# Kernel optimization log

Measured on AMD Instinct MI355X. Metric: run time of the kernel, lower is better.

Reference implementation:

```python
import jax, jax.numpy as jnp
import numpy as np

SIZE_DICT = 1024  # K
DIM_DICT = 256    # D


def setup_inputs() -> dict:
    key = jax.random.key(0)
    k1, k2, k3 = jax.random.split(key, 3)
    z = jax.random.normal(k1, (64, 1024, DIM_DICT), dtype=jnp.float32)
    codebook = jax.random.normal(k2, (SIZE_DICT, DIM_DICT), dtype=jnp.float32)
    codebook_weight = jax.random.normal(k3, (SIZE_DICT,), dtype=jnp.float32)
    return {
        "z_from_encoder": z,
        "codebook": codebook,
        "codebook_weight": codebook_weight,
        "flg_train": 0,
    }


def reference(z_from_encoder, codebook, codebook_weight, flg_train):
    z = z_from_encoder
    z_flat = z.reshape(-1, DIM_DICT)  # [N, D]
    # Pairwise squared distances: ||z||^2 + ||c||^2 - 2 z.c  -> [N, K]
    cost = (
        jnp.sum(z_flat ** 2, axis=1, keepdims=True)
        + jnp.sum(codebook ** 2, axis=1)
        - 2.0 * jnp.matmul(z_flat, codebook.T)
    )
    idx = jnp.argmin(cost, axis=1)  # [N]
    # one-hot scatter + matmul with codebook == gather of codebook rows
    z_q = codebook[idx].reshape(z.shape)
    # straight-through estimator
    z_q = z + jax.lax.stop_gradient(z_q - z)
    # loss is 0.0 in eval (flg_train False)
    loss = jnp.float32(0.0)
    # perplexity from mean one-hot encodings
    n = z_flat.shape[0]
    counts = jnp.zeros((SIZE_DICT,), dtype=jnp.float32).at[idx].add(1.0)
    e_mean = counts / n
    perplexity = jnp.exp(-jnp.sum(e_mean * jnp.log(e_mean + 1e-10)))
    return z_q, loss, perplexity
```

## Files before the change

### kernel.cpp

```cpp
#include <hip/hip_runtime.h>
#include <hip/hip_bf16.h>
#include <stdint.h>


typedef float  v4f __attribute__((ext_vector_type(4)));
typedef _Float16 v8h __attribute__((ext_vector_type(8)));
typedef _Float16 v4h __attribute__((ext_vector_type(4)));

#define N_ROWS 65536
#define N_DICT 1024
#define DIMS   256
#define MARGIN 4e-3f

__device__ __forceinline__ void gl_lds16(const void* g, void* l) {
  __builtin_amdgcn_global_load_lds(
      (const __attribute__((address_space(1))) unsigned int*)g,
      (__attribute__((address_space(3))) unsigned int*)l,
      16, 0, 0);
}

__global__ void k_prep(const float* __restrict__ cb, _Float16* __restrict__ swz_h,
                       _Float16* __restrict__ swz_l, float* __restrict__ cnA,
                       double* __restrict__ cnD,
                       unsigned* __restrict__ hist, unsigned* __restrict__ counters) {
  const int b = blockIdx.x, t = threadIdx.x;
  if (b == 0) {
    for (int i = t; i < N_DICT; i += 256) hist[i] = 0u;
    if (t == 0) { counters[0] = 0u; counters[1] = 0u; }
  }
  const int gid = b * 256 + t;
  const int col = gid >> 6;
  const int k0  = (gid & 63) * 4;
  v4f v = ((const v4f*)cb)[gid];
  v4h h, l;
  #pragma unroll
  for (int j = 0; j < 4; ++j) {
    h[j] = (_Float16)v[j];
    float r = v[j] - (float)h[j];
    l[j] = (_Float16)r;
  }
  const int c = col >> 6, t4 = (col >> 4) & 3, l15 = col & 15;
  const int kk = k0 >> 5, q = (k0 >> 3) & 3, j0 = k0 & 7;
  const size_t off = (size_t)(((c * 8 + kk) * 4 + t4) * 512 + (q * 16 + l15) * 8 + j0);
  *(v4h*)(swz_h + off) = h;
  *(v4h*)(swz_l + off) = l;
  const int lane = t & 63, w = t >> 6;
  const int row = b * 4 + w;
  v4f u = ((const v4f*)cb)[row * 64 + lane];
  double s = (double)u[0]*u[0] + (double)u[1]*u[1]
           + (double)u[2]*u[2] + (double)u[3]*u[3];
  #pragma unroll
  for (int d = 1; d < 64; d <<= 1) s += __shfl_xor(s, d);
  if (lane == 0) { cnA[row] = (float)s; cnD[row] = s; }
}

__launch_bounds__(512, 2)
__global__ void k_main(const float* __restrict__ z, const _Float16* __restrict__ swz_h,
                       const _Float16* __restrict__ swz_l, const float* __restrict__ cnA,
                       unsigned* __restrict__ out_idx,
                       unsigned long long* __restrict__ list1,
                       unsigned* __restrict__ list2,
                       unsigned* __restrict__ counters) {
  __shared__ __align__(16) char lds[4][32768];
  const int t = threadIdx.x, lane = t & 63, w = t >> 6;
  const int l15 = lane & 15, q = lane >> 4;
  const int waverow = (blockIdx.x * 8 + w) * 32;

  v8h ah[2][8], al[2][8];
  #pragma unroll
  for (int m = 0; m < 2; ++m) {
    const float* zp = z + (size_t)(waverow + m * 16 + l15) * DIMS + q * 8;
    #pragma unroll
    for (int kk = 0; kk < 8; ++kk) {
      v4f f0 = *(const v4f*)(zp + kk * 32);
      v4f f1 = *(const v4f*)(zp + kk * 32 + 4);
      v8h hh, ll;
      #pragma unroll
      for (int j = 0; j < 4; ++j) {
        hh[j] = (_Float16)f0[j];
        float r = f0[j] - (float)hh[j];
        ll[j] = (_Float16)r;
        hh[4 + j] = (_Float16)f1[j];
        r = f1[j] - (float)hh[4 + j];
        ll[4 + j] = (_Float16)r;
      }
      ah[m][kk] = hh; al[m][kk] = ll;
    }
  }

  const int s0 = w * 4;
  const char* gsrc_base = (const char*)(s0 >= 16 ? swz_l : swz_h);

  float m1[8], m2[8], m3[8]; int c1[8], c2[8];
  #pragma unroll
  for (int s = 0; s < 8; ++s) {
    m1[s] = 1e30f; m2[s] = 1e30f; m3[s] = 1e30f; c1[s] = 0; c2[s] = 0;
  }

  #pragma unroll
  for (int n = 0; n < 2; ++n) {
    const int c = n >> 1, half = n & 1;
    #pragma unroll
    for (int i = 0; i < 4; ++i) {
      const int s = s0 + i, kk = (s >> 1) & 7, u = s & 1;
      const char* gb = gsrc_base +
          (size_t)(c * 32768 + kk * 4096 + (2 * half + u) * 1024 + lane * 16);
      gl_lds16(gb, &lds[n][s * 1024]);
    }
  }

  for (int cc = 0; cc < 32; ++cc) {
    if (cc < 31) asm volatile("s_waitcnt vmcnt(4)" ::: "memory");
    else         asm volatile("s_waitcnt vmcnt(0)" ::: "memory");
    __builtin_amdgcn_s_barrier();
    __builtin_amdgcn_sched_barrier(0);

    if (cc <= 29) {
      const int n = cc + 2, c = n >> 1, half = n & 1;
      char* nbuf = lds[n & 3];
      #pragma unroll
      for (int i = 0; i < 4; ++i) {
        const int s = s0 + i, kk = (s >> 1) & 7, u = s & 1;
        const char* gb = gsrc_base +
            (size_t)(c * 32768 + kk * 4096 + (2 * half + u) * 1024 + lane * 16);
        gl_lds16(gb, nbuf + s * 1024);
      }
    }

    const char* buf = lds[cc & 3];
    const int c = cc >> 1, half = cc & 1;
    const int n0 = c * 64 + half * 32;
    float cn[2]; int colv[2];
    #pragma unroll
    for (int u = 0; u < 2; ++u) {
      colv[u] = n0 + u * 16 + l15;
      cn[u] = cnA[colv[u]];
    }
    v4f acc[2][2];
    #pragma unroll
    for (int m = 0; m < 2; ++m)
      #pragma unroll
      for (int u = 0; u < 2; ++u) acc[m][u] = (v4f){0.f, 0.f, 0.f, 0.f};

    #pragma unroll
    for (int kk = 0; kk < 8; ++kk) {
      v8h b_h[2], b_l[2];
      #pragma unroll
      for (int u = 0; u < 2; ++u)
        b_h[u] = *(const v8h*)(buf + (kk * 2 + u) * 1024 + lane * 16);
      #pragma unroll
      for (int u = 0; u < 2; ++u)
        b_l[u] = *(const v8h*)(buf + 16384 + (kk * 2 + u) * 1024 + lane * 16);
      #pragma unroll
      for (int m = 0; m < 2; ++m) {
        #pragma unroll
        for (int u = 0; u < 2; ++u)
          acc[m][u] = __builtin_amdgcn_mfma_f32_16x16x32_f16(ah[m][kk], b_h[u], acc[m][u], 0, 0, 0);
        #pragma unroll
        for (int u = 0; u < 2; ++u)
          acc[m][u] = __builtin_amdgcn_mfma_f32_16x16x32_f16(al[m][kk], b_h[u], acc[m][u], 0, 0, 0);
        #pragma unroll
        for (int u = 0; u < 2; ++u)
          acc[m][u] = __builtin_amdgcn_mfma_f32_16x16x32_f16(ah[m][kk], b_l[u], acc[m][u], 0, 0, 0);
      }
    }
    #pragma unroll
    for (int m = 0; m < 2; ++m)
      #pragma unroll
      for (int u = 0; u < 2; ++u)
        #pragma unroll
        for (int r = 0; r < 4; ++r) {
          float cost = fmaf(acc[m][u][r], -2.0f, cn[u]);
          const int s = m * 4 + r;
          bool lt1 = cost < m1[s];
          bool lt2 = cost < m2[s];
          bool lt3 = cost < m3[s];
          m3[s] = lt2 ? m2[s] : (lt3 ? cost : m3[s]);
          m2[s] = lt1 ? m1[s] : (lt2 ? cost : m2[s]);
          c2[s] = lt1 ? c1[s] : (lt2 ? colv[u] : c2[s]);
          m1[s] = lt1 ? cost : m1[s];
          c1[s] = lt1 ? colv[u] : c1[s];
        }
  }

  #pragma unroll
  for (int d = 1; d < 16; d <<= 1) {
    #pragma unroll
    for (int s = 0; s < 8; ++s) {
      float om1 = __shfl_xor(m1[s], d);
      float om2 = __shfl_xor(m2[s], d);
      float om3 = __shfl_xor(m3[s], d);
      int   oc1 = __shfl_xor(c1[s], d);
      int   oc2 = __shfl_xor(c2[s], d);
      bool take = (om1 < m1[s]) || (om1 == m1[s] && oc1 < c1[s]);
      float w1 = take ? om1 : m1[s];  int wc1 = take ? oc1 : c1[s];
      float w2 = take ? om2 : m2[s];  int wc2 = take ? oc2 : c2[s];
      float w3 = take ? om3 : m3[s];
      float l1 = take ? m1[s] : om1;  int lc1 = take ? c1[s] : oc1;
      float l2 = take ? m2[s] : om2;
      bool t2 = (l1 < w2) || (l1 == w2 && lc1 < wc2);
      m1[s] = w1; c1[s] = wc1;
      m2[s] = t2 ? l1 : w2;
      c2[s] = t2 ? lc1 : wc2;
      m3[s] = t2 ? fminf(w2, l2) : fminf(w3, l1);
    }
  }
  if (l15 < 8) {
    const int s = l15, m = s >> 2, r = s & 3;
    const int row = waverow + m * 16 + q * 4 + r;
    out_idx[row] = (unsigned)c1[s];
    if (m3[s] - m1[s] < MARGIN) {
      unsigned pos = atomicAdd(&counters[1], 1u);
      list2[pos] = (unsigned)row;
    } else if (m2[s] - m1[s] < MARGIN) {
      unsigned pos = atomicAdd(&counters[0], 1u);
      list1[pos] = (unsigned long long)row
                 | ((unsigned long long)(unsigned)c1[s] << 20)
                 | ((unsigned long long)(unsigned)c2[s] << 40);
    }
  }
}

__global__ void k_pair(const float* __restrict__ z, const float* __restrict__ cb,
                       const double* __restrict__ cnD,
                       const unsigned long long* __restrict__ list1,
                       const unsigned* __restrict__ counters,
                       unsigned* __restrict__ out_idx) {
  const unsigned count = counters[0];
  if (count == 0) return;
  const int t = threadIdx.x, lane = t & 63, w = t >> 6;
  const unsigned gw = blockIdx.x * 4 + w;
  const unsigned nw = gridDim.x * 4;
  const int half = lane >> 5, l5 = lane & 31;
  for (unsigned g = gw; g < count; g += nw) {
    const unsigned long long e = list1[g];
    const unsigned row = (unsigned)(e & 0xFFFFFu);
    const int c1 = (int)((e >> 20) & 0x3FFu);
    const int c2 = (int)((e >> 40) & 0x3FFu);
    const int col = half ? c2 : c1;
    const float* cp = cb + (size_t)col * DIMS + l5 * 8;
    const float* zr = z + (size_t)row * DIMS + l5 * 8;
    v4f z0 = *(const v4f*)zr,      z1 = *(const v4f*)(zr + 4);
    v4f cc0 = *(const v4f*)cp,     cc1 = *(const v4f*)(cp + 4);
    double a = (double)z0[0] * (double)cc0[0];
    a = fma((double)z0[1], (double)cc0[1], a);
    a = fma((double)z0[2], (double)cc0[2], a);
    a = fma((double)z0[3], (double)cc0[3], a);
    a = fma((double)z1[0], (double)cc1[0], a);
    a = fma((double)z1[1], (double)cc1[1], a);
    a = fma((double)z1[2], (double)cc1[2], a);
    a = fma((double)z1[3], (double)cc1[3], a);
    #pragma unroll
    for (int d = 1; d < 32; d <<= 1) a += __shfl_xor(a, d);
    double cost = cnD[col] - 2.0 * a;
    double oc = __shfl_xor(cost, 32);
    if (lane == 0) {
      bool take = (oc < cost) || (oc == cost && c2 < c1);
      out_idx[row] = take ? (unsigned)c2 : (unsigned)c1;
    }
  }
}

__global__ void k_deep(const float* __restrict__ z, const float* __restrict__ cb,
                       const double* __restrict__ cnD,
                       const unsigned* __restrict__ list2,
                       const unsigned* __restrict__ counters,
                       unsigned* __restrict__ out_idx) {
  const unsigned count = counters[1];
  if (count == 0) return;
  const int t = threadIdx.x, lane = t & 63, w = t >> 6;
  __shared__ double sc[4];
  __shared__ int scc[4];
  for (unsigned g = blockIdx.x; g < count; g += gridDim.x) {
    const unsigned row = list2[g];
    const float* zr = z + (size_t)row * DIMS;
    double best = 1e300; int bc = 1 << 30;
    for (int ci = w * 4; ci < w * 4 + 4; ++ci) {
      const int col = ci * 64 + lane;
      const float* cp = cb + (size_t)col * DIMS;
      double a0 = 0, a1 = 0, a2 = 0, a3 = 0, a4 = 0, a5 = 0, a6 = 0, a7 = 0;
      #pragma unroll 8
      for (int k = 0; k < DIMS; k += 8) {
        v4f z0 = *(const v4f*)(zr + k);
        v4f z1 = *(const v4f*)(zr + k + 4);
        v4f cc0 = *(const v4f*)(cp + k);
        v4f cc1 = *(const v4f*)(cp + k + 4);
        a0 = fma((double)z0[0], (double)cc0[0], a0);
        a1 = fma((double)z0[1], (double)cc0[1], a1);
        a2 = fma((double)z0[2], (double)cc0[2], a2);
        a3 = fma((double)z0[3], (double)cc0[3], a3);
        a4 = fma((double)z1[0], (double)cc1[0], a4);
        a5 = fma((double)z1[1], (double)cc1[1], a5);
        a6 = fma((double)z1[2], (double)cc1[2], a6);
        a7 = fma((double)z1[3], (double)cc1[3], a7);
      }
      double cost = cnD[col]
                  - 2.0 * (((a0 + a1) + (a2 + a3)) + ((a4 + a5) + (a6 + a7)));
      if (cost < best || (cost == best && col < bc)) { best = cost; bc = col; }
    }
    #pragma unroll
    for (int d = 1; d < 64; d <<= 1) {
      double ob = __shfl_xor(best, d);
      int    oc = __shfl_xor(bc, d);
      if (ob < best || (ob == best && oc < bc)) { best = ob; bc = oc; }
    }
    if (lane == 0) { sc[w] = best; scc[w] = bc; }
    __syncthreads();
    if (t == 0) {
      double b = sc[0]; int c = scc[0];
      #pragma unroll
      for (int i = 1; i < 4; ++i)
        if (sc[i] < b || (sc[i] == b && scc[i] < c)) { b = sc[i]; c = scc[i]; }
      out_idx[row] = (unsigned)c;
    }
    __syncthreads();
  }
}

__global__ void k_gather(const float* __restrict__ cb, const unsigned* __restrict__ idx,
                         float* __restrict__ outz, unsigned* __restrict__ hist) {
  const int t = threadIdx.x, lane = t & 63, w = t >> 6;
  const int base = (blockIdx.x * 4 + w) * 16;
  #pragma unroll 4
  for (int r = 0; r < 16; ++r) {
    const int row = base + r;
    const unsigned id = idx[row];
    v4f v = *(const v4f*)(cb + (size_t)id * DIMS + lane * 4);
    *(v4f*)(outz + (size_t)row * DIMS + lane * 4) = v;
    if (lane == (r & 63)) atomicAdd(hist + id, 1u);
  }
}

__global__ void k_stats(const unsigned* __restrict__ hist, float* __restrict__ out) {
  const int t = threadIdx.x;
  float s = 0.f;
  for (int i = t; i < N_DICT; i += 256) {
    float p = (float)hist[i] * (1.0f / (float)N_ROWS);
    s += p * logf(p + 1e-10f);
  }
  #pragma unroll
  for (int d = 1; d < 64; d <<= 1) s += __shfl_xor(s, d);
  __shared__ float ls[4];
  if ((t & 63) == 0) ls[t >> 6] = s;
  __syncthreads();
  if (t == 0) {
    float tot = ls[0] + ls[1] + ls[2] + ls[3];
    out[16777216] = 0.0f;
    out[16777217] = expf(-tot);
  }
}

extern "C" void kernel_launch(void* const* d_in, const int* in_sizes, int n_in,
                              void* d_out, int out_size, void* d_ws, size_t ws_size,
                              hipStream_t stream) {
  const float* z  = (const float*)d_in[0];
  const float* cb = (const float*)d_in[1];
  float* out = (float*)d_out;
  char* ws = (char*)d_ws;
  _Float16* swz_h            = (_Float16*)ws;
  _Float16* swz_l            = (_Float16*)(ws + 524288);
  float*    cnA              = (float*)(ws + 1048576);
  double*   cnD              = (double*)(ws + 1052672);
  unsigned* idx              = (unsigned*)(ws + 1060864);
  unsigned long long* list1  = (unsigned long long*)(ws + 1323008);
  unsigned* list2            = (unsigned*)(ws + 1847296);
  unsigned* hist             = (unsigned*)(ws + 2109440);
  unsigned* counters         = (unsigned*)(ws + 2113536);

  k_prep  <<<256,  256, 0, stream>>>(cb, swz_h, swz_l, cnA, cnD, hist, counters);
  k_main  <<<256,  512, 0, stream>>>(z, swz_h, swz_l, cnA, idx, list1, list2, counters);
  k_pair  <<<1024, 256, 0, stream>>>(z, cb, cnD, list1, counters, idx);
  k_deep  <<<2048, 256, 0, stream>>>(z, cb, cnD, list2, counters, idx);
  k_gather<<<1024, 256, 0, stream>>>(cb, idx, out, hist);
  k_stats <<<1,    256, 0, stream>>>(hist, out);
}
```

Before: 246.6 us.

## Use single-fp16 MFMA screening with norm-scaled error margin and merged resolve kernel

```diff
diff --git a/kernel.cpp b/kernel.cpp
--- a/kernel.cpp
+++ b/kernel.cpp
@@ -10,7 +10,6 @@
 #define N_ROWS 65536
 #define N_DICT 1024
 #define DIMS   256
-#define MARGIN 4e-3f
 
 __device__ __forceinline__ void gl_lds16(const void* g, void* l) {
   __builtin_amdgcn_global_load_lds(
@@ -20,30 +19,20 @@
 }
 
 __global__ void k_prep(const float* __restrict__ cb, _Float16* __restrict__ swz_h,
-                       _Float16* __restrict__ swz_l, float* __restrict__ cnA,
-                       double* __restrict__ cnD,
-                       unsigned* __restrict__ hist, unsigned* __restrict__ counters) {
+                       float* __restrict__ cnA, double* __restrict__ cnD,
+                       unsigned* __restrict__ counters) {
   const int b = blockIdx.x, t = threadIdx.x;
-  if (b == 0) {
-    for (int i = t; i < N_DICT; i += 256) hist[i] = 0u;
-    if (t == 0) { counters[0] = 0u; counters[1] = 0u; }
-  }
   const int gid = b * 256 + t;
   const int col = gid >> 6;
   const int k0  = (gid & 63) * 4;
   v4f v = ((const v4f*)cb)[gid];
-  v4h h, l;
-  #pragma unroll
-  for (int j = 0; j < 4; ++j) {
-    h[j] = (_Float16)v[j];
-    float r = v[j] - (float)h[j];
-    l[j] = (_Float16)r;
-  }
+  v4h h;
+  #pragma unroll
+  for (int j = 0; j < 4; ++j) h[j] = (_Float16)v[j];
   const int c = col >> 6, t4 = (col >> 4) & 3, l15 = col & 15;
   const int kk = k0 >> 5, q = (k0 >> 3) & 3, j0 = k0 & 7;
   const size_t off = (size_t)(((c * 8 + kk) * 4 + t4) * 512 + (q * 16 + l15) * 8 + j0);
   *(v4h*)(swz_h + off) = h;
-  *(v4h*)(swz_l + off) = l;
   const int lane = t & 63, w = t >> 6;
   const int row = b * 4 + w;
   v4f u = ((const v4f*)cb)[row * 64 + lane];
@@ -51,22 +40,31 @@
            + (double)u[2]*u[2] + (double)u[3]*u[3];
   #pragma unroll
   for (int d = 1; d < 64; d <<= 1) s += __shfl_xor(s, d);
-  if (lane == 0) { cnA[row] = (float)s; cnD[row] = s; }
+  if (lane == 0) {
+    float sf = (float)s;
+    cnA[row] = sf; cnD[row] = s;
+    atomicMax(&counters[2], __float_as_uint(sf));
+  }
 }
 
 __launch_bounds__(512, 2)
 __global__ void k_main(const float* __restrict__ z, const _Float16* __restrict__ swz_h,
-                       const _Float16* __restrict__ swz_l, const float* __restrict__ cnA,
+                       const float* __restrict__ cnA,
                        unsigned* __restrict__ out_idx,
                        unsigned long long* __restrict__ list1,
                        unsigned* __restrict__ list2,
                        unsigned* __restrict__ counters) {
   __shared__ __align__(16) char lds[4][32768];
+  __shared__ float lds_cn[N_DICT];
   const int t = threadIdx.x, lane = t & 63, w = t >> 6;
   const int l15 = lane & 15, q = lane >> 4;
   const int waverow = (blockIdx.x * 8 + w) * 32;
-
-  v8h ah[2][8], al[2][8];
+  const float cbmax2 = __uint_as_float(counters[2]);
+
+  for (int i = t; i < N_DICT; i += 512) lds_cn[i] = cnA[i];
+
+  v8h ah[2][8];
+  float norm2[2] = {0.f, 0.f};
   #pragma unroll
   for (int m = 0; m < 2; ++m) {
     const float* zp = z + (size_t)(waverow + m * 16 + l15) * DIMS + q * 8;
@@ -74,22 +72,20 @@
     for (int kk = 0; kk < 8; ++kk) {
       v4f f0 = *(const v4f*)(zp + kk * 32);
       v4f f1 = *(const v4f*)(zp + kk * 32 + 4);
-      v8h hh, ll;
+      v8h hh;
       #pragma unroll
       for (int j = 0; j < 4; ++j) {
-        hh[j] = (_Float16)f0[j];
-        float r = f0[j] - (float)hh[j];
-        ll[j] = (_Float16)r;
+        hh[j]     = (_Float16)f0[j];
         hh[4 + j] = (_Float16)f1[j];
-        r = f1[j] - (float)hh[4 + j];
-        ll[4 + j] = (_Float16)r;
-      }
-      ah[m][kk] = hh; al[m][kk] = ll;
-    }
+        norm2[m] += f0[j] * f0[j] + f1[j] * f1[j];
+      }
+      ah[m][kk] = hh;
+    }
+    norm2[m] += __shfl_xor(norm2[m], 16);
+    norm2[m] += __shfl_xor(norm2[m], 32);
   }
 
   const int s0 = w * 4;
-  const char* gsrc_base = (const char*)(s0 >= 16 ? swz_l : swz_h);
 
   float m1[8], m2[8], m3[8]; int c1[8], c2[8];
   #pragma unroll
@@ -98,88 +94,72 @@
   }
 
   #pragma unroll
-  for (int n = 0; n < 2; ++n) {
-    const int c = n >> 1, half = n & 1;
-    #pragma unroll
-    for (int i = 0; i < 4; ++i) {
-      const int s = s0 + i, kk = (s >> 1) & 7, u = s & 1;
-      const char* gb = gsrc_base +
-          (size_t)(c * 32768 + kk * 4096 + (2 * half + u) * 1024 + lane * 16);
-      gl_lds16(gb, &lds[n][s * 1024]);
-    }
-  }
-
-  for (int cc = 0; cc < 32; ++cc) {
-    if (cc < 31) asm volatile("s_waitcnt vmcnt(4)" ::: "memory");
-    else         asm volatile("s_waitcnt vmcnt(0)" ::: "memory");
+  for (int n = 0; n < 2; ++n)
+    #pragma unroll
+    for (int i = 0; i < 4; ++i)
+      gl_lds16(swz_h + (size_t)n * 16384 + (size_t)(s0 + i) * 512 + lane * 8,
+               &lds[n][(s0 + i) * 1024]);
+  __syncthreads();
+
+  for (int cc = 0; cc < 16; ++cc) {
+    if (cc >= 2) {
+      if (cc < 15) asm volatile("s_waitcnt vmcnt(4)" ::: "memory");
+      else         asm volatile("s_waitcnt vmcnt(0)" ::: "memory");
+    }
     __builtin_amdgcn_s_barrier();
     __builtin_amdgcn_sched_barrier(0);
 
-    if (cc <= 29) {
-      const int n = cc + 2, c = n >> 1, half = n & 1;
+    if (cc <= 13) {
+      const int n = cc + 2;
       char* nbuf = lds[n & 3];
       #pragma unroll
-      for (int i = 0; i < 4; ++i) {
-        const int s = s0 + i, kk = (s >> 1) & 7, u = s & 1;
-        const char* gb = gsrc_base +
-            (size_t)(c * 32768 + kk * 4096 + (2 * half + u) * 1024 + lane * 16);
-        gl_lds16(gb, nbuf + s * 1024);
-      }
+      for (int i = 0; i < 4; ++i)
+        gl_lds16(swz_h + (size_t)n * 16384 + (size_t)(s0 + i) * 512 + lane * 8,
+                 nbuf + (s0 + i) * 1024);
     }
 
     const char* buf = lds[cc & 3];
-    const int c = cc >> 1, half = cc & 1;
-    const int n0 = c * 64 + half * 32;
-    float cn[2]; int colv[2];
-    #pragma unroll
-    for (int u = 0; u < 2; ++u) {
-      colv[u] = n0 + u * 16 + l15;
-      cn[u] = cnA[colv[u]];
-    }
-    v4f acc[2][2];
+    const int n0 = cc * 64;
+    float cn[4]; int colv[4];
+    #pragma unroll
+    for (int t4 = 0; t4 < 4; ++t4) {
+      colv[t4] = n0 + t4 * 16 + l15;
+      cn[t4] = lds_cn[colv[t4]];
+    }
+    v4f acc[2][4];
     #pragma unroll
     for (int m = 0; m < 2; ++m)
       #pragma unroll
-      for (int u = 0; u < 2; ++u) acc[m][u] = (v4f){0.f, 0.f, 0.f, 0.f};
+      for (int t4 = 0; t4 < 4; ++t4) acc[m][t4] = (v4f){0.f, 0.f, 0.f, 0.f};
 
     #pragma unroll
     for (int kk = 0; kk < 8; ++kk) {
-      v8h b_h[2], b_l[2];
-      #pragma unroll
-      for (int u = 0; u < 2; ++u)
-        b_h[u] = *(const v8h*)(buf + (kk * 2 + u) * 1024 + lane * 16);
-      #pragma unroll
-      for (int u = 0; u < 2; ++u)
-        b_l[u] = *(const v8h*)(buf + 16384 + (kk * 2 + u) * 1024 + lane * 16);
-      #pragma unroll
-      for (int m = 0; m < 2; ++m) {
+      v8h b_h[4];
+      #pragma unroll
+      for (int t4 = 0; t4 < 4; ++t4)
+        b_h[t4] = *(const v8h*)(buf + (kk * 4 + t4) * 1024 + lane * 16);
+      #pragma unroll
+      for (int m = 0; m < 2; ++m)
         #pragma unroll
-        for (int u = 0; u < 2; ++u)
-          acc[m][u] = __builtin_amdgcn_mfma_f32_16x16x32_f16(ah[m][kk], b_h[u], acc[m][u], 0, 0, 0);
-        #pragma unroll
-        for (int u = 0; u < 2; ++u)
-          acc[m][u] = __builtin_amdgcn_mfma_f32_16x16x32_f16(al[m][kk], b_h[u], acc[m][u], 0, 0, 0);
-        #pragma unroll
-        for (int u = 0; u < 2; ++u)
-          acc[m][u] = __builtin_amdgcn_mfma_f32_16x16x32_f16(ah[m][kk], b_l[u], acc[m][u], 0, 0, 0);
-      }
+        for (int t4 = 0; t4 < 4; ++t4)
+          acc[m][t4] = __builtin_amdgcn_mfma_f32_16x16x32_f16(ah[m][kk], b_h[t4], acc[m][t4], 0, 0, 0);
     }
     #pragma unroll
     for (int m = 0; m < 2; ++m)
       #pragma unroll
-      for (int u = 0; u < 2; ++u)
+      for (int t4 = 0; t4 < 4; ++t4)
         #pragma unroll
         for (int r = 0; r < 4; ++r) {
-          float cost = fmaf(acc[m][u][r], -2.0f, cn[u]);
+          float cost = fmaf(acc[m][t4][r], -2.0f, cn[t4]);
           const int s = m * 4 + r;
           bool lt1 = cost < m1[s];
           bool lt2 = cost < m2[s];
           bool lt3 = cost < m3[s];
           m3[s] = lt2 ? m2[s] : (lt3 ? cost : m3[s]);
           m2[s] = lt1 ? m1[s] : (lt2 ? cost : m2[s]);
-          c2[s] = lt1 ? c1[s] : (lt2 ? colv[u] : c2[s]);
+          c2[s] = lt1 ? c1[s] : (lt2 ? colv[t4] : c2[s]);
           m1[s] = lt1 ? cost : m1[s];
-          c1[s] = lt1 ? colv[u] : c1[s];
+          c1[s] = lt1 ? colv[t4] : c1[s];
         }
   }
 
@@ -205,14 +185,18 @@
       m3[s] = t2 ? fminf(w2, l2) : fminf(w3, l1);
     }
   }
+  float nza = __shfl(norm2[0], q * 4 + (l15 & 3));
+  float nzb = __shfl(norm2[1], q * 4 + (l15 & 3));
   if (l15 < 8) {
     const int s = l15, m = s >> 2, r = s & 3;
     const int row = waverow + m * 16 + q * 4 + r;
+    const float nzr = m ? nzb : nza;
+    const float M = 0.004023f * sqrtf(nzr * cbmax2) + 1e-3f;
     out_idx[row] = (unsigned)c1[s];
-    if (m3[s] - m1[s] < MARGIN) {
+    if (m3[s] - m1[s] < M) {
       unsigned pos = atomicAdd(&counters[1], 1u);
       list2[pos] = (unsigned)row;
-    } else if (m2[s] - m1[s] < MARGIN) {
+    } else if (m2[s] - m1[s] < M) {
       unsigned pos = atomicAdd(&counters[0], 1u);
       list1[pos] = (unsigned long long)row
                  | ((unsigned long long)(unsigned)c1[s] << 20)
@@ -221,99 +205,94 @@
   }
 }
 
-__global__ void k_pair(const float* __restrict__ z, const float* __restrict__ cb,
-                       const double* __restrict__ cnD,
-                       const unsigned long long* __restrict__ list1,
-                       const unsigned* __restrict__ counters,
-                       unsigned* __restrict__ out_idx) {
-  const unsigned count = counters[0];
-  if (count == 0) return;
+__global__ void k_resolve(const float* __restrict__ z, const float* __restrict__ cb,
+                          const double* __restrict__ cnD,
+                          const unsigned long long* __restrict__ list1,
+                          const unsigned* __restrict__ list2,
+                          const unsigned* __restrict__ counters,
+                          unsigned* __restrict__ out_idx) {
   const int t = threadIdx.x, lane = t & 63, w = t >> 6;
-  const unsigned gw = blockIdx.x * 4 + w;
-  const unsigned nw = gridDim.x * 4;
-  const int half = lane >> 5, l5 = lane & 31;
-  for (unsigned g = gw; g < count; g += nw) {
-    const unsigned long long e = list1[g];
-    const unsigned row = (unsigned)(e & 0xFFFFFu);
-    const int c1 = (int)((e >> 20) & 0x3FFu);
-    const int c2 = (int)((e >> 40) & 0x3FFu);
-    const int col = half ? c2 : c1;
-    const float* cp = cb + (size_t)col * DIMS + l5 * 8;
-    const float* zr = z + (size_t)row * DIMS + l5 * 8;
-    v4f z0 = *(const v4f*)zr,      z1 = *(const v4f*)(zr + 4);
-    v4f cc0 = *(const v4f*)cp,     cc1 = *(const v4f*)(cp + 4);
-    double a = (double)z0[0] * (double)cc0[0];
-    a = fma((double)z0[1], (double)cc0[1], a);
-    a = fma((double)z0[2], (double)cc0[2], a);
-    a = fma((double)z0[3], (double)cc0[3], a);
-    a = fma((double)z1[0], (double)cc1[0], a);
-    a = fma((double)z1[1], (double)cc1[1], a);
-    a = fma((double)z1[2], (double)cc1[2], a);
-    a = fma((double)z1[3], (double)cc1[3], a);
-    #pragma unroll
-    for (int d = 1; d < 32; d <<= 1) a += __shfl_xor(a, d);
-    double cost = cnD[col] - 2.0 * a;
-    double oc = __shfl_xor(cost, 32);
-    if (lane == 0) {
-      bool take = (oc < cost) || (oc == cost && c2 < c1);
-      out_idx[row] = take ? (unsigned)c2 : (unsigned)c1;
-    }
-  }
-}
-
-__global__ void k_deep(const float* __restrict__ z, const float* __restrict__ cb,
-                       const double* __restrict__ cnD,
-                       const unsigned* __restrict__ list2,
-                       const unsigned* __restrict__ counters,
-                       unsigned* __restrict__ out_idx) {
-  const unsigned count = counters[1];
-  if (count == 0) return;
-  const int t = threadIdx.x, lane = t & 63, w = t >> 6;
-  __shared__ double sc[4];
-  __shared__ int scc[4];
-  for (unsigned g = blockIdx.x; g < count; g += gridDim.x) {
-    const unsigned row = list2[g];
-    const float* zr = z + (size_t)row * DIMS;
-    double best = 1e300; int bc = 1 << 30;
-    for (int ci = w * 4; ci < w * 4 + 4; ++ci) {
-      const int col = ci * 64 + lane;
-      const float* cp = cb + (size_t)col * DIMS;
-      double a0 = 0, a1 = 0, a2 = 0, a3 = 0, a4 = 0, a5 = 0, a6 = 0, a7 = 0;
-      #pragma unroll 8
-      for (int k = 0; k < DIMS; k += 8) {
-        v4f z0 = *(const v4f*)(zr + k);
-        v4f z1 = *(const v4f*)(zr + k + 4);
-        v4f cc0 = *(const v4f*)(cp + k);
-        v4f cc1 = *(const v4f*)(cp + k + 4);
-        a0 = fma((double)z0[0], (double)cc0[0], a0);
-        a1 = fma((double)z0[1], (double)cc0[1], a1);
-        a2 = fma((double)z0[2], (double)cc0[2], a2);
-        a3 = fma((double)z0[3], (double)cc0[3], a3);
-        a4 = fma((double)z1[0], (double)cc1[0], a4);
-        a5 = fma((double)z1[1], (double)cc1[1], a5);
-        a6 = fma((double)z1[2], (double)cc1[2], a6);
-        a7 = fma((double)z1[3], (double)cc1[3], a7);
-      }
-      double cost = cnD[col]
-                  - 2.0 * (((a0 + a1) + (a2 + a3)) + ((a4 + a5) + (a6 + a7)));
-      if (cost < best || (cost == best && col < bc)) { best = cost; bc = col; }
-    }
-    #pragma unroll
-    for (int d = 1; d < 64; d <<= 1) {
-      double ob = __shfl_xor(best, d);
-      int    oc = __shfl_xor(bc, d);
-      if (ob < best || (ob == best && oc < bc)) { best = ob; bc = oc; }
-    }
-    if (lane == 0) { sc[w] = best; scc[w] = bc; }
-    __syncthreads();
-    if (t == 0) {
-      double b = sc[0]; int c = scc[0];
-      #pragma unroll
-      for (int i = 1; i < 4; ++i)
-        if (sc[i] < b || (sc[i] == b && scc[i] < c)) { b = sc[i]; c = scc[i]; }
-      out_idx[row] = (unsigned)c;
-    }
-    __syncthreads();
+  if (blockIdx.x < 1024) {
+    const unsigned count = counters[0];
+    if (count == 0) return;
+    const unsigned gw = blockIdx.x * 4 + w;
+    const int half = lane >> 5, l5 = lane & 31;
+    for (unsigned g = gw; g < count; g += 4096) {
+      const unsigned long long e = list1[g];
+      const unsigned row = (unsigned)(e & 0xFFFFFu);
+      const int c1 = (int)((e >> 20) & 0x3FFu);
+      const int c2 = (int)((e >> 40) & 0x3FFu);
+      const int col = half ? c2 : c1;
+      const float* cp = cb + (size_t)col * DIMS + l5 * 8;
+      const float* zr = z + (size_t)row * DIMS + l5 * 8;
+      v4f z0 = *(const v4f*)zr,  z1 = *(const v4f*)(zr + 4);
+      v4f cc0 = *(const v4f*)cp, cc1 = *(const v4f*)(cp + 4);
+      double a = (double)z0[0] * (double)cc0[0];
+      a = fma((double)z0[1], (double)cc0[1], a);
+      a = fma((double)z0[2], (double)cc0[2], a);
+      a = fma((double)z0[3], (double)cc0[3], a);
+      a = fma((double)z1[0], (double)cc1[0], a);
+      a = fma((double)z1[1], (double)cc1[1], a);
+      a = fma((double)z1[2], (double)cc1[2], a);
+      a = fma((double)z1[3], (double)cc1[3], a);
+      #pragma unroll
+      for (int d = 1; d < 32; d <<= 1) a += __shfl_xor(a, d);
+      double cost = cnD[col] - 2.0 * a;
+      double oc = __shfl_xor(cost, 32);
+      if (lane == 0) {
+        bool take = (oc < cost) || (oc == cost && c2 < c1);
+        out_idx[row] = take ? (unsigned)c2 : (unsigned)c1;
+      }
+    }
+  } else {
+    const unsigned count = counters[1];
+    if (count == 0) return;
+    __shared__ double sc[4];
+    __shared__ int scc[4];
+    for (unsigned g = blockIdx.x - 1024; g < count; g += 2048) {
+      const unsigned row = list2[g];
+      const float* zr = z + (size_t)row * DIMS;
+      double best = 1e300; int bc = 1 << 30;
+      for (int ci = w * 4; ci < w * 4 + 4; ++ci) {
+        const int col = ci * 64 + lane;
+        const float* cp = cb + (size_t)col * DIMS;
+        double a0 = 0, a1 = 0, a2 = 0, a3 = 0, a4 = 0, a5 = 0, a6 = 0, a7 = 0;
+        #pragma unroll 8
+        for (int k = 0; k < DIMS; k += 8) {
+          v4f z0 = *(const v4f*)(zr + k);
+          v4f z1 = *(const v4f*)(zr + k + 4);
+          v4f cc0 = *(const v4f*)(cp + k);
+          v4f cc1 = *(const v4f*)(cp + k + 4);
+          a0 = fma((double)z0[0], (double)cc0[0], a0);
+          a1 = fma((double)z0[1], (double)cc0[1], a1);
+          a2 = fma((double)z0[2], (double)cc0[2], a2);
+          a3 = fma((double)z0[3], (double)cc0[3], a3);
+          a4 = fma((double)z1[0], (double)cc1[0], a4);
+          a5 = fma((double)z1[1], (double)cc1[1], a5);
+          a6 = fma((double)z1[2], (double)cc1[2], a6);
+          a7 = fma((double)z1[3], (double)cc1[3], a7);
+        }
+        double cost = cnD[col]
+                    - 2.0 * (((a0 + a1) + (a2 + a3)) + ((a4 + a5) + (a6 + a7)));
+        if (cost < best || (cost == best && col < bc)) { best = cost; bc = col; }
+      }
+      #pragma unroll
+      for (int d = 1; d < 64; d <<= 1) {
+        double ob = __shfl_xor(best, d);
+        int    oc = __shfl_xor(bc, d);
+        if (ob < best || (ob == best && oc < bc)) { best = ob; bc = oc; }
+      }
+      if (lane == 0) { sc[w] = best; scc[w] = bc; }
+      __syncthreads();
+      if (t == 0) {
+        double b = sc[0]; int c = scc[0];
+        #pragma unroll
+        for (int i = 1; i < 4; ++i)
+          if (sc[i] < b || (sc[i] == b && scc[i] < c)) { b = sc[i]; c = scc[i]; }
+        out_idx[row] = (unsigned)c;
+      }
+      __syncthreads();
+    }
   }
 }
 
@@ -358,19 +337,19 @@
   float* out = (float*)d_out;
   char* ws = (char*)d_ws;
   _Float16* swz_h            = (_Float16*)ws;
-  _Float16* swz_l            = (_Float16*)(ws + 524288);
-  float*    cnA              = (float*)(ws + 1048576);
-  double*   cnD              = (double*)(ws + 1052672);
-  unsigned* idx              = (unsigned*)(ws + 1060864);
-  unsigned long long* list1  = (unsigned long long*)(ws + 1323008);
-  unsigned* list2            = (unsigned*)(ws + 1847296);
-  unsigned* hist             = (unsigned*)(ws + 2109440);
-  unsigned* counters         = (unsigned*)(ws + 2113536);
-
-  k_prep  <<<256,  256, 0, stream>>>(cb, swz_h, swz_l, cnA, cnD, hist, counters);
-  k_main  <<<256,  512, 0, stream>>>(z, swz_h, swz_l, cnA, idx, list1, list2, counters);
-  k_pair  <<<1024, 256, 0, stream>>>(z, cb, cnD, list1, counters, idx);
-  k_deep  <<<2048, 256, 0, stream>>>(z, cb, cnD, list2, counters, idx);
-  k_gather<<<1024, 256, 0, stream>>>(cb, idx, out, hist);
-  k_stats <<<1,    256, 0, stream>>>(hist, out);
-}
+  float*    cnA              = (float*)(ws + 524288);
+  double*   cnD              = (double*)(ws + 528384);
+  unsigned* idx              = (unsigned*)(ws + 536576);
+  unsigned long long* list1  = (unsigned long long*)(ws + 798720);
+  unsigned* list2            = (unsigned*)(ws + 1323008);
+  unsigned* hist             = (unsigned*)(ws + 1585152);
+  unsigned* counters         = (unsigned*)(ws + 1589248);
+
+  hipMemsetAsync(hist, 0, 4096, stream);
+  hipMemsetAsync(counters, 0, 12, stream);
+  k_prep   <<<256,  256, 0, stream>>>(cb, swz_h, cnA, cnD, counters);
+  k_main   <<<256,  512, 0, stream>>>(z, swz_h, cnA, idx, list1, list2, counters);
+  k_resolve<<<3072, 256, 0, stream>>>(z, cb, cnD, list1, list2, counters, idx);
+  k_gather <<<1024, 256, 0, stream>>>(cb, idx, out, hist);
+  k_stats  <<<1,    256, 0, stream>>>(hist, out);
+}
```

New measurement: 362.9 us. 1.47x slower.
